# Kernel tuning notes

Measured on AMD Instinct MI355X. Metric: run time of the kernel, lower is better.

Reference implementation:

```python
import jax, jax.numpy as jnp
import numpy as np

B, N, IN_DIM, DIM, HEADS = 2, 4096, 1024, 1024, 8
MAX_MASK = 2048
SCALE = DIM ** -0.5  # original uses full dim, not per-head dim


def setup_inputs() -> dict:
    key = jax.random.key(0)
    k_x, k_qkv, k_o, k_b, k_m = jax.random.split(key, 5)
    x = jax.random.normal(k_x, (B, N, IN_DIM), dtype=jnp.float32)
    W_qkv = jax.random.normal(k_qkv, (IN_DIM, 3 * DIM), dtype=jnp.float32) * 0.02
    W_out = jax.random.normal(k_o, (DIM, DIM), dtype=jnp.float32) * 0.02
    b_out = jax.random.normal(k_b, (DIM,), dtype=jnp.float32) * 0.02
    mask = jax.random.randint(k_m, (1, 1, MAX_MASK, MAX_MASK), 0, 2, dtype=jnp.int32)
    return {"x": x, "W_qkv": W_qkv, "W_out": W_out, "b_out": b_out,
            "mask": mask, "max_mask": MAX_MASK}


def reference(x, W_qkv, W_out, b_out, mask, max_mask):
    b, n, _ = x.shape
    d = DIM // HEADS
    qkv = x @ W_qkv                                   # [b, n, 3*dim]
    qkv = qkv.reshape(b, n, 3, HEADS, d).transpose(2, 0, 3, 1, 4)  # [3, b, h, n, d]
    q, k, v = qkv[0], qkv[1], qkv[2]
    dots = jnp.einsum('bhid,bhjd->bhij', q, k) * SCALE  # [b, h, n, n]
    # partial submatrix masking on the top-left [max_mask, max_mask] block
    m = max_mask
    sub = jnp.where(mask == 0, -jnp.inf, dots[:, :, :m, :m])
    dots = dots.at[:, :, :m, :m].set(sub)
    attn = jax.nn.softmax(dots, axis=-1)
    out = jnp.einsum('bhij,bhjd->bhid', attn, v)       # [b, h, n, d]
    out = out.transpose(0, 2, 1, 3).reshape(b, n, HEADS * d)
    return out @ W_out + b_out
```

## Files before the change

kernel.cpp:

```cpp
#include <hip/hip_runtime.h>
#include <hip/hip_bf16.h>
#include <stdint.h>


typedef __attribute__((ext_vector_type(8))) short short8;
typedef __attribute__((ext_vector_type(4))) float f32x4;

#define SCALE_Q 0.03125f

__device__ __forceinline__ unsigned short f2bf(float f) {
  union { float f; unsigned int u; } v;
  v.f = f;
  return (unsigned short)((v.u + 0x7fffu + ((v.u >> 16) & 1u)) >> 16);
}

__device__ __forceinline__ unsigned int pkbf2(float a, float b) {
  __hip_bfloat162 h = __float22bfloat162_rn(make_float2(a, b));
  union { __hip_bfloat162 h; unsigned int u; } c;
  c.h = h;
  return c.u;
}

__device__ __forceinline__ void gload_lds16(const void* g, void* l) {
  __builtin_amdgcn_global_load_lds(
      (const __attribute__((address_space(1))) uint32_t*)(uintptr_t)g,
      (__attribute__((address_space(3))) uint32_t*)(uintptr_t)l, 16, 0, 0);
}

__device__ __forceinline__ f32x4 zero4() {
  f32x4 z; z.x = 0.f; z.y = 0.f; z.z = 0.f; z.w = 0.f; return z;
}

__global__ __launch_bounds__(256) void k_cvt_x(const float* __restrict__ in,
                                               unsigned short* __restrict__ out) {
  const int t = blockIdx.x * 256 + threadIdx.x;
  const float4 v = ((const float4*)in)[t];
  ushort4 o;
  o.x = f2bf(v.x); o.y = f2bf(v.y); o.z = f2bf(v.z); o.w = f2bf(v.w);
  ((ushort4*)out)[t] = o;
}

__global__ __launch_bounds__(256) void k_cvt_wt(const float* __restrict__ w,
                                                unsigned short* __restrict__ wt,
                                                int Nn) {
  __shared__ float t[32][33];
  const int n0 = blockIdx.x << 5, k0 = blockIdx.y << 5;
  const int c = threadIdx.x & 31, r8 = threadIdx.x >> 5;
#pragma unroll
  for (int i = 0; i < 4; ++i) {
    const int r = (i << 3) + r8;
    t[r][c] = w[(long)(k0 + r) * Nn + n0 + c];
  }
  __syncthreads();
#pragma unroll
  for (int i = 0; i < 4; ++i) {
    const int r = (i << 3) + r8;
    wt[(long)(n0 + r) * 1024 + k0 + c] = f2bf(t[c][r]);
  }
}

__global__ __launch_bounds__(256, 2) void k_qkv_gemm(
    const unsigned short* __restrict__ A,
    const unsigned short* __restrict__ Bt,
    unsigned short* __restrict__ Qs, unsigned short* __restrict__ Ks,
    unsigned short* __restrict__ Vs) {
  __shared__ __align__(16) unsigned short lA[4][128][8];
  __shared__ __align__(16) unsigned short lB[4][128][8];
  const int tid = threadIdx.x;
  const int w = tid >> 6, ln = tid & 63;
  const int m15 = ln & 15, q4 = ln >> 4;
  const int wm = (w >> 1) << 6, wn = (w & 1) << 6;
  const int tn = blockIdx.x, tm = blockIdx.y;

  f32x4 acc[4][4];
#pragma unroll
  for (int i = 0; i < 4; ++i)
#pragma unroll
    for (int j = 0; j < 4; ++j) acc[i][j] = zero4();

  for (int kb = 0; kb < 1024; kb += 32) {
    __syncthreads();
#pragma unroll
    for (int c = 0; c < 2; ++c) {
      const int p = ((c * 4 + w) << 10) + (ln << 4);
      const int g = p >> 11;
      const int r = (p & 2047) >> 4;
      gload_lds16(A + ((long)tm * 128 + r) * 1024 + kb + g * 8,
                  (char*)&lA[0][0][0] + p);
      gload_lds16(Bt + ((long)tn * 128 + r) * 1024 + kb + g * 8,
                  (char*)&lB[0][0][0] + p);
    }
    __syncthreads();
    short8 afr[4], bfr[4];
#pragma unroll
    for (int i = 0; i < 4; ++i)
      afr[i] = *(const short8*)&lA[q4][wm + i * 16 + m15][0];
#pragma unroll
    for (int j = 0; j < 4; ++j)
      bfr[j] = *(const short8*)&lB[q4][wn + j * 16 + m15][0];
#pragma unroll
    for (int i = 0; i < 4; ++i)
#pragma unroll
      for (int j = 0; j < 4; ++j)
        acc[i][j] = __builtin_amdgcn_mfma_f32_16x16x32_bf16(afr[i], bfr[j],
                                                            acc[i][j], 0, 0, 0);
  }

  const int which = tn >> 3;
  const int h = tn & 7;
#pragma unroll
  for (int i = 0; i < 4; ++i) {
#pragma unroll
    for (int r = 0; r < 4; ++r) {
      const int m = (tm << 7) + wm + (i << 4) + (q4 << 2) + r;
      const int b = m >> 12, row = m & 4095;
      const long bh = b * 8 + h;
#pragma unroll
      for (int j = 0; j < 4; ++j) {
        const int dd = wn + (j << 4) + m15;
        const float val = acc[i][j][r];
        if (which == 0)
          Qs[(bh * 4096 + row) * 128 + dd] = f2bf(val * SCALE_Q);
        else if (which == 1)
          Ks[(bh * 4096 + row) * 128 + dd] = f2bf(val);
        else
          Vs[(bh * 4096 + row) * 128 + dd] = f2bf(val);
      }
    }
  }
}

__global__ __launch_bounds__(256) void k_vtrans(
    const unsigned short* __restrict__ Vs, unsigned short* __restrict__ Vt) {
  __shared__ unsigned short t[64][66];
  const int n0 = blockIdx.x << 6, d0 = blockIdx.y << 6, bh = blockIdx.z;
  const int tt = threadIdx.x;
  const int nr = tt >> 2, dc = (tt & 3) << 4;
  const unsigned short* src = Vs + (((long)bh * 4096 + n0 + nr) << 7) + d0 + dc;
  *(short8*)&t[nr][dc] = *(const short8*)src;
  *(short8*)&t[nr][dc + 8] = *(const short8*)(src + 8);
  __syncthreads();
  const int dr = tt >> 2, nc = (tt & 3) << 4;
  short8 a, b;
#pragma unroll
  for (int jj = 0; jj < 8; ++jj) a[jj] = (short)t[nc + jj][dr];
#pragma unroll
  for (int jj = 0; jj < 8; ++jj) b[jj] = (short)t[nc + 8 + jj][dr];
  unsigned short* dst = Vt + (((long)bh * 128 + d0 + dr) << 12) + n0 + nc;
  *(short8*)dst = a;
  *(short8*)(dst + 8) = b;
}

__global__ __launch_bounds__(256, 2) void k_flash(
    const unsigned short* __restrict__ Qs, const unsigned short* __restrict__ Ks,
    const unsigned short* __restrict__ Vt, const int* __restrict__ mask,
    unsigned short* __restrict__ Ob) {
  __shared__ __align__(16) unsigned short lK[16][64][8];
  __shared__ __align__(16) unsigned short lV[8][128][8];
  __shared__ __align__(16) unsigned short lP[4][32][72];

  const int tid = threadIdx.x;
  const int w = tid >> 6, ln = tid & 63;
  const int m15 = ln & 15, q4 = ln >> 4;
  const int bh = blockIdx.y;
  const int rowblk = blockIdx.x;
  const int rbase = rowblk * 128 + w * 32;

  const unsigned short* Qbh = Qs + (long)bh * 524288;
  const unsigned short* Kbh = Ks + (long)bh * 524288;
  const unsigned short* Vbh = Vt + (long)bh * 524288;

  short8 qf[2][4];
#pragma unroll
  for (int i = 0; i < 2; ++i)
#pragma unroll
    for (int kk = 0; kk < 4; ++kk)
      qf[i][kk] = *(const short8*)(Qbh +
          (long)(rbase + i * 16 + m15) * 128 + kk * 32 + q4 * 8);

  f32x4 o[2][8];
#pragma unroll
  for (int i = 0; i < 2; ++i)
#pragma unroll
    for (int j = 0; j < 8; ++j) o[i][j] = zero4();
  f32x4 lacc[2];
  lacc[0] = zero4(); lacc[1] = zero4();

  const bool maskrows = rowblk < 16;

  for (int kv = 0; kv < 4096; kv += 64) {
    __syncthreads();
#pragma unroll
    for (int c = 0; c < 4; ++c) {
      const int p = ((c * 4 + w) << 10) + (ln << 4);
      const int cs = p >> 10;
      const int j = (p & 1023) >> 4;
      gload_lds16(Kbh + (long)(kv + j) * 128 + cs * 8, (char*)&lK[0][0][0] + p);
      const int cv = p >> 11;
      const int dv = (p & 2047) >> 4;
      gload_lds16(Vbh + (long)dv * 4096 + kv + cv * 8, (char*)&lV[0][0][0] + p);
    }
    __syncthreads();

    f32x4 s[2][4];
#pragma unroll
    for (int i = 0; i < 2; ++i)
#pragma unroll
      for (int jt = 0; jt < 4; ++jt) s[i][jt] = zero4();
#pragma unroll
    for (int jt = 0; jt < 4; ++jt) {
      short8 kfr[4];
#pragma unroll
      for (int kk = 0; kk < 4; ++kk)
        kfr[kk] = *(const short8*)&lK[kk * 4 + q4][jt * 16 + m15][0];
#pragma unroll
      for (int i = 0; i < 2; ++i)
#pragma unroll
        for (int kk = 0; kk < 4; ++kk)
          s[i][jt] = __builtin_amdgcn_mfma_f32_16x16x32_bf16(kfr[kk], qf[i][kk],
                                                             s[i][jt], 0, 0, 0);
    }

    if (maskrows && kv < 2048) {
#pragma unroll
      for (int i = 0; i < 2; ++i) {
        const int qrow = rbase + i * 16 + m15;
#pragma unroll
        for (int jt = 0; jt < 4; ++jt) {
          const int4 mv =
              *(const int4*)&mask[(long)qrow * 2048 + kv + jt * 16 + q4 * 4];
          s[i][jt].x = mv.x ? s[i][jt].x : -1e30f;
          s[i][jt].y = mv.y ? s[i][jt].y : -1e30f;
          s[i][jt].z = mv.z ? s[i][jt].z : -1e30f;
          s[i][jt].w = mv.w ? s[i][jt].w : -1e30f;
        }
      }
    }

#pragma unroll
    for (int i = 0; i < 2; ++i) {
#pragma unroll
      for (int jt = 0; jt < 4; ++jt) {
        f32x4 p;
        p.x = __expf(s[i][jt].x); p.y = __expf(s[i][jt].y);
        p.z = __expf(s[i][jt].z); p.w = __expf(s[i][jt].w);
        lacc[i].x += p.x; lacc[i].y += p.y;
        lacc[i].z += p.z; lacc[i].w += p.w;
        uint2 u;
        u.x = pkbf2(p.x, p.y);
        u.y = pkbf2(p.z, p.w);
        *(uint2*)&lP[w][i * 16 + m15][jt * 16 + q4 * 4] = u;
      }
    }
    __asm__ volatile("s_waitcnt lgkmcnt(0)" ::: "memory");

#pragma unroll
    for (int kk2 = 0; kk2 < 2; ++kk2) {
      short8 pf[2];
#pragma unroll
      for (int i = 0; i < 2; ++i)
        pf[i] = *(const short8*)&lP[w][i * 16 + m15][kk2 * 32 + q4 * 8];
#pragma unroll
      for (int jt2 = 0; jt2 < 8; ++jt2) {
        const short8 vf = *(const short8*)&lV[kk2 * 4 + q4][jt2 * 16 + m15][0];
#pragma unroll
        for (int i = 0; i < 2; ++i)
          o[i][jt2] = __builtin_amdgcn_mfma_f32_16x16x32_bf16(pf[i], vf,
                                                              o[i][jt2], 0, 0, 0);
      }
    }
  }

  const int b = bh >> 3, h = bh & 7;
#pragma unroll
  for (int i = 0; i < 2; ++i) {
    float lh = lacc[i].x + lacc[i].y + lacc[i].z + lacc[i].w;
    lh += __shfl_xor(lh, 16);
    lh += __shfl_xor(lh, 32);
    const float linv = 1.0f / lh;
    float linv_r[4];
#pragma unroll
    for (int r = 0; r < 4; ++r) linv_r[r] = __shfl(linv, q4 * 4 + r);
#pragma unroll
    for (int r = 0; r < 4; ++r) {
      const int row = rbase + i * 16 + q4 * 4 + r;
      unsigned short* op = Ob + ((long)(b * 4096 + row)) * 1024 + h * 128;
#pragma unroll
      for (int jt2 = 0; jt2 < 8; ++jt2)
        op[jt2 * 16 + m15] = f2bf(o[i][jt2][r] * linv_r[r]);
    }
  }
}

__global__ __launch_bounds__(256, 2) void k_proj_gemm(
    const unsigned short* __restrict__ A,
    const unsigned short* __restrict__ Bt,
    const float* __restrict__ bias, float* __restrict__ Out) {
  __shared__ __align__(16) unsigned short lA[4][128][8];
  __shared__ __align__(16) unsigned short lB[4][128][8];
  const int tid = threadIdx.x;
  const int w = tid >> 6, ln = tid & 63;
  const int m15 = ln & 15, q4 = ln >> 4;
  const int wm = (w >> 1) << 6, wn = (w & 1) << 6;
  const int tn = blockIdx.x, tm = blockIdx.y;

  f32x4 acc[4][4];
#pragma unroll
  for (int i = 0; i < 4; ++i)
#pragma unroll
    for (int j = 0; j < 4; ++j) acc[i][j] = zero4();

  for (int kb = 0; kb < 1024; kb += 32) {
    __syncthreads();
#pragma unroll
    for (int c = 0; c < 2; ++c) {
      const int p = ((c * 4 + w) << 10) + (ln << 4);
      const int g = p >> 11;
      const int r = (p & 2047) >> 4;
      gload_lds16(A + ((long)tm * 128 + r) * 1024 + kb + g * 8,
                  (char*)&lA[0][0][0] + p);
      gload_lds16(Bt + ((long)tn * 128 + r) * 1024 + kb + g * 8,
                  (char*)&lB[0][0][0] + p);
    }
    __syncthreads();
    short8 afr[4], bfr[4];
#pragma unroll
    for (int i = 0; i < 4; ++i)
      afr[i] = *(const short8*)&lA[q4][wm + i * 16 + m15][0];
#pragma unroll
    for (int j = 0; j < 4; ++j)
      bfr[j] = *(const short8*)&lB[q4][wn + j * 16 + m15][0];
#pragma unroll
    for (int i = 0; i < 4; ++i)
#pragma unroll
      for (int j = 0; j < 4; ++j)
        acc[i][j] = __builtin_amdgcn_mfma_f32_16x16x32_bf16(afr[i], bfr[j],
                                                            acc[i][j], 0, 0, 0);
  }

#pragma unroll
  for (int i = 0; i < 4; ++i)
#pragma unroll
    for (int r = 0; r < 4; ++r) {
      const int m = (tm << 7) + wm + (i << 4) + (q4 << 2) + r;
#pragma unroll
      for (int j = 0; j < 4; ++j) {
        const int n = (tn << 7) + wn + (j << 4) + m15;
        Out[(long)m * 1024 + n] = acc[i][j][r] + bias[n];
      }
    }
}

extern "C" void kernel_launch(void* const* d_in, const int* in_sizes, int n_in,
                              void* d_out, int out_size, void* d_ws,
                              size_t ws_size, hipStream_t stream) {
  const float* x = (const float*)d_in[0];
  const float* Wqkv = (const float*)d_in[1];
  const float* Wout = (const float*)d_in[2];
  const float* bout = (const float*)d_in[3];
  const int* mask = (const int*)d_in[4];
  float* out = (float*)d_out;

  char* ws = (char*)d_ws;
  unsigned short* xb     = (unsigned short*)(ws);
  unsigned short* wqkv_t = (unsigned short*)(ws + 16777216);
  unsigned short* wout_t = (unsigned short*)(ws + 23068672);
  unsigned short* Qs     = (unsigned short*)(ws + 25165824);
  unsigned short* Ks     = (unsigned short*)(ws + 41943040);
  unsigned short* Vt     = (unsigned short*)(ws + 58720256);
  unsigned short* Vs     = (unsigned short*)(ws + 75497472);
  unsigned short* Ob     = xb;

  hipLaunchKernelGGL(k_cvt_x, dim3(8192), dim3(256), 0, stream, x, xb);
  hipLaunchKernelGGL(k_cvt_wt, dim3(96, 32), dim3(256), 0, stream, Wqkv, wqkv_t, 3072);
  hipLaunchKernelGGL(k_cvt_wt, dim3(32, 32), dim3(256), 0, stream, Wout, wout_t, 1024);
  hipLaunchKernelGGL(k_qkv_gemm, dim3(24, 64), dim3(256), 0, stream,
                     xb, wqkv_t, Qs, Ks, Vs);
  hipLaunchKernelGGL(k_vtrans, dim3(64, 2, 16), dim3(256), 0, stream, Vs, Vt);
  hipLaunchKernelGGL(k_flash, dim3(32, 16), dim3(256), 0, stream,
                     Qs, Ks, Vt, mask, Ob);
  hipLaunchKernelGGL(k_proj_gemm, dim3(8, 64), dim3(256), 0, stream,
                     Ob, wout_t, bout, out);
}
```

Measured before the change: 487.0 us.

## Split flash attention over two KV halves and add a combine kernel

The flash attention kernel now splits the 4096-long KV range into two halves, each handled by a separate block. Each block now uses 512 threads covering 256 query rows, so every K/V tile staged in LDS is shared by twice as many rows. Each half writes its unnormalized partial output in bf16 plus per-row sums of exp values. A new elementwise combine kernel adds the two partials and normalizes, writing into the reused workspace. This is meant to raise wave-level parallelism and cut redundant K/V loads, at the cost of an extra kernel, extra partial-output traffic, and an added bf16 rounding of the unnormalized partials.

```diff
diff --git a/kernel.cpp b/kernel.cpp
--- a/kernel.cpp
+++ b/kernel.cpp
@@ -12,6 +12,12 @@
   union { float f; unsigned int u; } v;
   v.f = f;
   return (unsigned short)((v.u + 0x7fffu + ((v.u >> 16) & 1u)) >> 16);
+}
+
+__device__ __forceinline__ float bf2f(unsigned short h) {
+  union { unsigned int u; float f; } v;
+  v.u = ((unsigned int)h) << 16;
+  return v.f;
 }
 
 __device__ __forceinline__ unsigned int pkbf2(float a, float b) {
@@ -151,24 +157,25 @@
   *(short8*)(dst + 8) = b;
 }
 
-__global__ __launch_bounds__(256, 2) void k_flash(
+__global__ __launch_bounds__(512, 4) void k_flash(
     const unsigned short* __restrict__ Qs, const unsigned short* __restrict__ Ks,
     const unsigned short* __restrict__ Vt, const int* __restrict__ mask,
-    unsigned short* __restrict__ Ob) {
+    unsigned short* __restrict__ Op0, unsigned short* __restrict__ Op1,
+    float* __restrict__ Lp) {
   __shared__ __align__(16) unsigned short lK[16][64][8];
   __shared__ __align__(16) unsigned short lV[8][128][8];
-  __shared__ __align__(16) unsigned short lP[4][32][72];
+  __shared__ __align__(16) unsigned short lP[8][32][72];
 
   const int tid = threadIdx.x;
   const int w = tid >> 6, ln = tid & 63;
   const int m15 = ln & 15, q4 = ln >> 4;
-  const int bh = blockIdx.y;
-  const int rowblk = blockIdx.x;
-  const int rbase = rowblk * 128 + w * 32;
+  const int rowblk = blockIdx.x, kvs = blockIdx.y, bh = blockIdx.z;
+  const int rbase = rowblk * 256 + w * 32;
 
   const unsigned short* Qbh = Qs + (long)bh * 524288;
   const unsigned short* Kbh = Ks + (long)bh * 524288;
   const unsigned short* Vbh = Vt + (long)bh * 524288;
+  unsigned short* Op = kvs ? Op1 : Op0;
 
   short8 qf[2][4];
 #pragma unroll
@@ -186,16 +193,21 @@
   f32x4 lacc[2];
   lacc[0] = zero4(); lacc[1] = zero4();
 
-  const bool maskrows = rowblk < 16;
-
-  for (int kv = 0; kv < 4096; kv += 64) {
-    __syncthreads();
-#pragma unroll
-    for (int c = 0; c < 4; ++c) {
-      const int p = ((c * 4 + w) << 10) + (ln << 4);
+  const bool maskblk = (rowblk < 8) && (kvs == 0);
+  const int kv0 = kvs << 11;
+
+  for (int kv = kv0; kv < kv0 + 2048; kv += 64) {
+    __syncthreads();
+#pragma unroll
+    for (int c = 0; c < 2; ++c) {
+      const int p = ((c * 8 + w) << 10) + (ln << 4);
       const int cs = p >> 10;
       const int j = (p & 1023) >> 4;
       gload_lds16(Kbh + (long)(kv + j) * 128 + cs * 8, (char*)&lK[0][0][0] + p);
+    }
+#pragma unroll
+    for (int c = 0; c < 2; ++c) {
+      const int p = ((c * 8 + w) << 10) + (ln << 4);
       const int cv = p >> 11;
       const int dv = (p & 2047) >> 4;
       gload_lds16(Vbh + (long)dv * 4096 + kv + cv * 8, (char*)&lV[0][0][0] + p);
@@ -221,7 +233,7 @@
                                                              s[i][jt], 0, 0, 0);
     }
 
-    if (maskrows && kv < 2048) {
+    if (maskblk) {
 #pragma unroll
       for (int i = 0; i < 2; ++i) {
         const int qrow = rbase + i * 16 + m15;
@@ -277,19 +289,36 @@
     float lh = lacc[i].x + lacc[i].y + lacc[i].z + lacc[i].w;
     lh += __shfl_xor(lh, 16);
     lh += __shfl_xor(lh, 32);
-    const float linv = 1.0f / lh;
-    float linv_r[4];
-#pragma unroll
-    for (int r = 0; r < 4; ++r) linv_r[r] = __shfl(linv, q4 * 4 + r);
+    if (ln < 16)
+      Lp[(((long)kvs * 16 + bh) << 12) + rbase + i * 16 + m15] = lh;
 #pragma unroll
     for (int r = 0; r < 4; ++r) {
       const int row = rbase + i * 16 + q4 * 4 + r;
-      unsigned short* op = Ob + ((long)(b * 4096 + row)) * 1024 + h * 128;
+      unsigned short* op = Op + ((long)(b * 4096 + row)) * 1024 + h * 128;
 #pragma unroll
       for (int jt2 = 0; jt2 < 8; ++jt2)
-        op[jt2 * 16 + m15] = f2bf(o[i][jt2][r] * linv_r[r]);
-    }
-  }
+        op[jt2 * 16 + m15] = f2bf(o[i][jt2][r]);
+    }
+  }
+}
+
+__global__ __launch_bounds__(256) void k_combine(
+    const unsigned short* __restrict__ O0, const unsigned short* __restrict__ O1,
+    const float* __restrict__ Lp, unsigned short* __restrict__ Ob) {
+  const long t = (long)blockIdx.x * 256 + threadIdx.x;
+  const long idx = t << 3;
+  const int m = (int)(idx >> 10), col = (int)(idx & 1023);
+  const int b = m >> 12, row = m & 4095, h = col >> 7;
+  const long li = (((long)(b * 8 + h)) << 12) + row;
+  const float linv = 1.0f / (Lp[li] + Lp[li + (16L << 12)]);
+  const short8 a = *(const short8*)(O0 + idx);
+  const short8 c = *(const short8*)(O1 + idx);
+  short8 o;
+#pragma unroll
+  for (int k = 0; k < 8; ++k)
+    o[k] = (short)f2bf((bf2f((unsigned short)a[k]) +
+                        bf2f((unsigned short)c[k])) * linv);
+  *(short8*)(Ob + idx) = o;
 }
 
 __global__ __launch_bounds__(256, 2) void k_proj_gemm(
@@ -369,7 +398,11 @@
   unsigned short* Ks     = (unsigned short*)(ws + 41943040);
   unsigned short* Vt     = (unsigned short*)(ws + 58720256);
   unsigned short* Vs     = (unsigned short*)(ws + 75497472);
-  unsigned short* Ob     = xb;
+
+  unsigned short* Op0 = xb;
+  unsigned short* Op1 = Vs;
+  float*          Lp  = (float*)wqkv_t;
+  unsigned short* Ob  = Qs;
 
   hipLaunchKernelGGL(k_cvt_x, dim3(8192), dim3(256), 0, stream, x, xb);
   hipLaunchKernelGGL(k_cvt_wt, dim3(96, 32), dim3(256), 0, stream, Wqkv, wqkv_t, 3072);
@@ -377,8 +410,10 @@
   hipLaunchKernelGGL(k_qkv_gemm, dim3(24, 64), dim3(256), 0, stream,
                      xb, wqkv_t, Qs, Ks, Vs);
   hipLaunchKernelGGL(k_vtrans, dim3(64, 2, 16), dim3(256), 0, stream, Vs, Vt);
-  hipLaunchKernelGGL(k_flash, dim3(32, 16), dim3(256), 0, stream,
-                     Qs, Ks, Vt, mask, Ob);
+  hipLaunchKernelGGL(k_flash, dim3(16, 2, 16), dim3(512), 0, stream,
+                     Qs, Ks, Vt, mask, Op0, Op1, Lp);
+  hipLaunchKernelGGL(k_combine, dim3(4096), dim3(256), 0, stream,
+                     Op0, Op1, Lp, Ob);
   hipLaunchKernelGGL(k_proj_gemm, dim3(8, 64), dim3(256), 0, stream,
                      Ob, wout_t, bout, out);
 }
```

Result: slower. 1.041 ms (+113.8%).
